# Optimization experiments

Measured on AMD Instinct MI355X. Metric: run time of the kernel, lower is better.

## Reference

```python
import jax, jax.numpy as jnp
import numpy as np
import math

N_HEAD = 16
N_KV_HEAD = 4
N_EMBD = 2048
HEAD_DIM = N_EMBD // N_HEAD  # 128
SCALE = 1.0 / math.sqrt(HEAD_DIM)
B, T = 2, 2048


def setup_inputs() -> dict:
    key = jax.random.key(0)
    ks = jax.random.split(key, 5)
    s = 0.02
    x = jax.random.normal(ks[0], (B, T, N_EMBD), dtype=jnp.float32)
    wq = jax.random.normal(ks[1], (N_EMBD, N_EMBD), dtype=jnp.float32) * s
    wk = jax.random.normal(ks[2], (N_KV_HEAD * HEAD_DIM, N_EMBD), dtype=jnp.float32) * s
    wv = jax.random.normal(ks[3], (N_KV_HEAD * HEAD_DIM, N_EMBD), dtype=jnp.float32) * s
    wo = jax.random.normal(ks[4], (N_EMBD, N_EMBD), dtype=jnp.float32) * s
    return {"x": x, "wq": wq, "wk": wk, "wv": wv, "wo": wo}


def _forward(x, wq, wk, wv, wo):
    b, t, _ = x.shape
    # Linear layers: y = x @ W.T  (torch Linear weight is (out,in))
    q = (x @ wq.T).reshape(b, t, N_HEAD, HEAD_DIM).transpose(0, 2, 1, 3)      # (B,H,T,D)
    k = (x @ wk.T).reshape(b, t, N_KV_HEAD, HEAD_DIM).transpose(0, 2, 1, 3)  # (B,Hkv,T,D)
    v = (x @ wv.T).reshape(b, t, N_KV_HEAD, HEAD_DIM).transpose(0, 2, 1, 3)
    groups = N_HEAD // N_KV_HEAD
    k = jnp.repeat(k, groups, axis=1)  # repeat_interleave over head dim -> (B,H,T,D)
    v = jnp.repeat(v, groups, axis=1)
    # Causal mask: True above diagonal (masked-out positions)
    mask = jnp.triu(jnp.ones((t, t), dtype=bool), k=1)[None, None]  # (1,1,T,T)
    scores = jnp.einsum('bhqd,bhkd->bhqk', q, k) * SCALE
    scores = jnp.where(mask, -jnp.inf, scores)
    attn = jax.nn.softmax(scores, axis=-1)
    attn = jnp.where(mask, 0.0, attn)
    y = jnp.einsum('bhqk,bhkd->bhqd', attn, v)       # (B,H,T,D)
    y = y.transpose(0, 2, 1, 3).reshape(b, t, N_EMBD)
    return y @ wo.T


def reference(x, wq, wk, wv, wo):
    return _forward(x, wq, wk, wv, wo)
```

## Files before the change

kernel.cpp:

```cpp
#include <hip/hip_runtime.h>
#include <cstdint>
#include <cstddef>

typedef __bf16 bf16_t;
typedef __bf16 bf16x8 __attribute__((ext_vector_type(8)));
typedef __bf16 bf16x4 __attribute__((ext_vector_type(4)));
typedef float f32x4 __attribute__((ext_vector_type(4)));

#define GL2LDS16(gptr, lptr)                                                   \
  __builtin_amdgcn_global_load_lds(                                            \
      (__attribute__((address_space(1))) void*)(gptr),                         \
      (__attribute__((address_space(3))) void*)(lptr), 16, 0, 0)

__device__ __forceinline__ float fast_exp2(float x) {
  float r;
  asm volatile("v_exp_f32 %0, %1" : "=v"(r) : "v"(x));
  return r;
}

#define BATCH 2
#define T_SEQ 2048
#define NH 16
#define NKV 4
#define HD 128
#define EMB 2048
#define KVDIM (NKV * HD)
#define MROWS (BATCH * T_SEQ)

__global__ void cvt_all(const float4* __restrict__ x,  const float4* __restrict__ wq,
                        const float4* __restrict__ wk, const float4* __restrict__ wv,
                        const float4* __restrict__ wo,
                        bf16x4* __restrict__ xb,  bf16x4* __restrict__ wqb,
                        bf16x4* __restrict__ wkb, bf16x4* __restrict__ wvb,
                        bf16x4* __restrict__ wob) {
  const int blk = blockIdx.x;
  const float4* src;
  bf16x4* dst;
  int base;
  if (blk < 8192)       { src = x;  dst = xb;  base = blk; }
  else if (blk < 12288) { src = wq; dst = wqb; base = blk - 8192; }
  else if (blk < 13312) { src = wk; dst = wkb; base = blk - 12288; }
  else if (blk < 14336) { src = wv; dst = wvb; base = blk - 13312; }
  else                  { src = wo; dst = wob; base = blk - 14336; }
  const int i = base * 256 + threadIdx.x;
  const float4 v = src[i];
  dst[i] = bf16x4{(__bf16)v.x, (__bf16)v.y, (__bf16)v.z, (__bf16)v.w};
}

__global__ __launch_bounds__(256, 2)
void gemm_qkv(const bf16_t* __restrict__ A,
              const bf16_t* __restrict__ Wq, const bf16_t* __restrict__ Wk,
              const bf16_t* __restrict__ Wv,
              bf16_t* __restrict__ Qb, bf16_t* __restrict__ Kb,
              bf16_t* __restrict__ Vt, float qalpha)
{
  __shared__ bf16_t As[128 * 64];
  __shared__ bf16_t Bs[128 * 64];

  const int tid  = threadIdx.x;
  const int lane = tid & 63;
  const int wv   = tid >> 6;
  const int nbx = blockIdx.x;
  const int m0 = blockIdx.y * 128;
  const int wm = (wv >> 1) * 64;
  const int wn = (wv & 1) * 64;
  const int l15 = lane & 15;
  const int lq  = lane >> 4;

  const bf16_t* Bm;
  int ncol0;
  if (nbx < 16)      { Bm = Wq; ncol0 = nbx * 128; }
  else if (nbx < 20) { Bm = Wk; ncol0 = (nbx - 16) * 128; }
  else               { Bm = Wv; ncol0 = (nbx - 20) * 128; }

  f32x4 acc[4][4] = {};
  const int srow = tid >> 3;
  const int scol = (tid & 7) * 8;

  for (int k0 = 0; k0 < EMB; k0 += 64) {
#pragma unroll
    for (int r = 0; r < 4; ++r) {
      const int row = r * 32 + srow;
      GL2LDS16(A + (size_t)(m0 + row) * EMB + k0 + scol, As + row * 64 + scol);
    }
#pragma unroll
    for (int r = 0; r < 4; ++r) {
      const int row = r * 32 + srow;
      GL2LDS16(Bm + (size_t)(ncol0 + row) * EMB + k0 + scol, Bs + row * 64 + scol);
    }
    __syncthreads();

#pragma unroll
    for (int ks = 0; ks < 2; ++ks) {
      const int kc = ks * 32 + lq * 8;
      bf16x8 af[4], bf[4];
#pragma unroll
      for (int i = 0; i < 4; ++i)
        af[i] = *(const bf16x8*)(As + (wm + i * 16 + l15) * 64 + kc);
#pragma unroll
      for (int j = 0; j < 4; ++j)
        bf[j] = *(const bf16x8*)(Bs + (wn + j * 16 + l15) * 64 + kc);
#pragma unroll
      for (int i = 0; i < 4; ++i)
#pragma unroll
        for (int j = 0; j < 4; ++j)
          acc[i][j] = __builtin_amdgcn_mfma_f32_16x16x32_bf16(af[i], bf[j], acc[i][j], 0, 0, 0);
    }
    __syncthreads();
  }

  if (nbx < 16) {
#pragma unroll
    for (int i = 0; i < 4; ++i) {
      const int rbase = m0 + wm + i * 16 + lq * 4;
#pragma unroll
      for (int j = 0; j < 4; ++j) {
        const int col = ncol0 + wn + j * 16 + l15;
#pragma unroll
        for (int r = 0; r < 4; ++r)
          Qb[(size_t)(rbase + r) * EMB + col] = (bf16_t)(acc[i][j][r] * qalpha);
      }
    }
  } else if (nbx < 20) {
#pragma unroll
    for (int i = 0; i < 4; ++i) {
      const int rbase = m0 + wm + i * 16 + lq * 4;
#pragma unroll
      for (int j = 0; j < 4; ++j) {
        const int col = ncol0 + wn + j * 16 + l15;
#pragma unroll
        for (int r = 0; r < 4; ++r)
          Kb[(size_t)(rbase + r) * KVDIM + col] = (bf16_t)acc[i][j][r];
      }
    }
  } else {
    const int b = m0 >> 11;
    const int mloc0 = (m0 & 2047) + wm + lq * 4;
#pragma unroll
    for (int i = 0; i < 4; ++i) {
      const int mloc = mloc0 + i * 16;
#pragma unroll
      for (int j = 0; j < 4; ++j) {
        const int d = ncol0 + wn + j * 16 + l15;
        *(bf16x4*)(Vt + (size_t)(b * KVDIM + d) * T_SEQ + mloc) =
            bf16x4{(__bf16)acc[i][j][0], (__bf16)acc[i][j][1],
                   (__bf16)acc[i][j][2], (__bf16)acc[i][j][3]};
      }
    }
  }
}

__global__ __launch_bounds__(256, 2)
void gemm_out(const bf16_t* __restrict__ A, const bf16_t* __restrict__ Bm,
              float* __restrict__ C, int M, int N, int K)
{
  __shared__ bf16_t As[128 * 64];
  __shared__ bf16_t Bs[128 * 64];

  const int tid  = threadIdx.x;
  const int lane = tid & 63;
  const int wv   = tid >> 6;
  const int m0 = blockIdx.y * 128;
  const int n0 = blockIdx.x * 128;
  const int wm = (wv >> 1) * 64;
  const int wn = (wv & 1) * 64;
  const int l15 = lane & 15;
  const int lq  = lane >> 4;

  f32x4 acc[4][4] = {};
  const int srow = tid >> 3;
  const int scol = (tid & 7) * 8;

  for (int k0 = 0; k0 < K; k0 += 64) {
#pragma unroll
    for (int r = 0; r < 4; ++r) {
      const int row = r * 32 + srow;
      GL2LDS16(A + (size_t)(m0 + row) * K + k0 + scol, As + row * 64 + scol);
    }
#pragma unroll
    for (int r = 0; r < 4; ++r) {
      const int row = r * 32 + srow;
      GL2LDS16(Bm + (size_t)(n0 + row) * K + k0 + scol, Bs + row * 64 + scol);
    }
    __syncthreads();

#pragma unroll
    for (int ks = 0; ks < 2; ++ks) {
      const int kc = ks * 32 + lq * 8;
      bf16x8 af[4], bf[4];
#pragma unroll
      for (int i = 0; i < 4; ++i)
        af[i] = *(const bf16x8*)(As + (wm + i * 16 + l15) * 64 + kc);
#pragma unroll
      for (int j = 0; j < 4; ++j)
        bf[j] = *(const bf16x8*)(Bs + (wn + j * 16 + l15) * 64 + kc);
#pragma unroll
      for (int i = 0; i < 4; ++i)
#pragma unroll
        for (int j = 0; j < 4; ++j)
          acc[i][j] = __builtin_amdgcn_mfma_f32_16x16x32_bf16(af[i], bf[j], acc[i][j], 0, 0, 0);
    }
    __syncthreads();
  }

#pragma unroll
  for (int i = 0; i < 4; ++i) {
    const int rbase = m0 + wm + i * 16 + lq * 4;
#pragma unroll
    for (int j = 0; j < 4; ++j) {
      const int col = n0 + wn + j * 16 + l15;
#pragma unroll
      for (int r = 0; r < 4; ++r)
        C[(size_t)(rbase + r) * N + col] = acc[i][j][r];
    }
  }
}

#define PSTR 72

__global__ __launch_bounds__(256, 2)
void attn_fwd(const bf16_t* __restrict__ Q, const bf16_t* __restrict__ Kg,
              const bf16_t* __restrict__ Vt, bf16_t* __restrict__ Y)
{
  __shared__ bf16_t Ks[2][64 * 128];
  __shared__ bf16_t Vs[2][128 * 64];
  __shared__ bf16_t Ps[4][16 * PSTR];

  const int tid  = threadIdx.x;
  const int lane = tid & 63;
  const int wv   = tid >> 6;
  const int l15  = lane & 15;
  const int lq   = lane >> 4;
  const int h  = blockIdx.y;
  const int b  = blockIdx.z;
  const int hkv = h >> 2;
  bf16_t* Psw = Ps[wv];

  auto stage = [&](int kt, int bufsel) {
    const int base_t = b * T_SEQ + kt * 64;
#pragma unroll
    for (int r = 0; r < 4; ++r) {
      const int c = r * 256 + tid;
      const int row = c >> 4, p = c & 15;
      const int sb = p ^ (row & 7);
      GL2LDS16(Kg + (size_t)(base_t + row) * KVDIM + hkv * HD + sb * 8,
               &Ks[bufsel][c * 8]);
    }
#pragma unroll
    for (int r = 0; r < 4; ++r) {
      const int c = r * 256 + tid;
      const int row = c >> 3, p = c & 7;
      const int sb = p ^ (row & 7);
      GL2LDS16(Vt + (size_t)(b * KVDIM + hkv * HD + row) * T_SEQ + kt * 64 + sb * 8,
               &Vs[bufsel][c * 8]);
    }
  };

#pragma unroll 1
  for (int ph = 0; ph < 2; ++ph) {
    const int qt = ph ? blockIdx.x : (31 - blockIdx.x);
    const int q0 = qt * 64;
    const int nkt = qt + 1;
    const int qabs = q0 + wv * 16 + l15;

    bf16x8 qf[4];
    {
      const bf16_t* qp = Q + ((size_t)(b * T_SEQ + qabs) * NH + h) * HD + lq * 8;
#pragma unroll
      for (int ds = 0; ds < 4; ++ds)
        qf[ds] = *(const bf16x8*)(qp + ds * 32);
    }

    float l_part = 0.f;
    f32x4 o[8];
#pragma unroll
    for (int nb = 0; nb < 8; ++nb) o[nb] = f32x4{0.f, 0.f, 0.f, 0.f};

    __syncthreads();
    stage(0, 0);

    for (int kt = 0; kt < nkt; ++kt) {
      const int cur = kt & 1;
      __syncthreads();
      if (kt + 1 < nkt) stage(kt + 1, cur ^ 1);

      f32x4 s[4];
#pragma unroll
      for (int nb = 0; nb < 4; ++nb) {
        s[nb] = f32x4{0.f, 0.f, 0.f, 0.f};
        const int row = nb * 16 + l15;
        const int r7  = row & 7;
#pragma unroll
        for (int ds = 0; ds < 4; ++ds) {
          const bf16x8 kf = *(const bf16x8*)&Ks[cur][row * 128 + (((ds * 4 + lq) ^ r7) * 8)];
          s[nb] = __builtin_amdgcn_mfma_f32_16x16x32_bf16(kf, qf[ds], s[nb], 0, 0, 0);
        }
      }

      const bool dia = (kt == nkt - 1);
#pragma unroll
      for (int nb = 0; nb < 4; ++nb) {
        const int kvb = kt * 64 + nb * 16 + lq * 4;
        float p0, p1, p2, p3;
        if (dia) {
          p0 = (kvb + 0 <= qabs) ? fast_exp2(s[nb][0]) : 0.f;
          p1 = (kvb + 1 <= qabs) ? fast_exp2(s[nb][1]) : 0.f;
          p2 = (kvb + 2 <= qabs) ? fast_exp2(s[nb][2]) : 0.f;
          p3 = (kvb + 3 <= qabs) ? fast_exp2(s[nb][3]) : 0.f;
        } else {
          p0 = fast_exp2(s[nb][0]);
          p1 = fast_exp2(s[nb][1]);
          p2 = fast_exp2(s[nb][2]);
          p3 = fast_exp2(s[nb][3]);
        }
        l_part += (p0 + p1) + (p2 + p3);
        *(bf16x4*)(Psw + l15 * PSTR + nb * 16 + lq * 4) =
            bf16x4{(__bf16)p0, (__bf16)p1, (__bf16)p2, (__bf16)p3};
      }

      asm volatile("s_waitcnt lgkmcnt(0)" ::: "memory");

#pragma unroll
      for (int ks = 0; ks < 2; ++ks) {
        const bf16x8 pf = *(const bf16x8*)(Psw + l15 * PSTR + ks * 32 + lq * 8);
#pragma unroll
        for (int nb = 0; nb < 8; ++nb) {
          const int row = nb * 16 + l15;
          const bf16x8 vf = *(const bf16x8*)&Vs[cur][row * 64 + (((ks * 4 + lq) ^ (row & 7)) * 8)];
          o[nb] = __builtin_amdgcn_mfma_f32_16x16x32_bf16(vf, pf, o[nb], 0, 0, 0);
        }
      }
    }

    float lt = l_part;
    lt += __shfl_xor(lt, 16);
    lt += __shfl_xor(lt, 32);
    const float inv = 1.f / lt;
    bf16_t* yp = Y + ((size_t)(b * T_SEQ + qabs) * NH + h) * HD + lq * 4;
#pragma unroll
    for (int nb = 0; nb < 8; ++nb) {
      *(bf16x4*)(yp + nb * 16) = bf16x4{(__bf16)(o[nb][0] * inv), (__bf16)(o[nb][1] * inv),
                                        (__bf16)(o[nb][2] * inv), (__bf16)(o[nb][3] * inv)};
    }
  }
}

extern "C" void kernel_launch(void* const* d_in, const int* in_sizes, int n_in,
                              void* d_out, int out_size, void* d_ws, size_t ws_size,
                              hipStream_t stream) {
  const float* x  = (const float*)d_in[0];
  const float* wq = (const float*)d_in[1];
  const float* wk = (const float*)d_in[2];
  const float* wv = (const float*)d_in[3];
  const float* wo = (const float*)d_in[4];
  float* out = (float*)d_out;

  const size_t n_x  = (size_t)MROWS * EMB;
  const size_t n_wq = (size_t)EMB * EMB;
  const size_t n_wk = (size_t)KVDIM * EMB;

  bf16_t* xb  = (bf16_t*)d_ws;
  bf16_t* wqb = xb  + n_x;
  bf16_t* wkb = wqb + n_wq;
  bf16_t* wvb = wkb + n_wk;
  bf16_t* wob = wvb + n_wk;
  bf16_t* Qb  = wob + n_wq;
  bf16_t* Kb  = Qb + (size_t)MROWS * EMB;
  bf16_t* Vtb = Kb + (size_t)MROWS * KVDIM;
  bf16_t* Yb  = Vtb + (size_t)MROWS * KVDIM;

  dim3 blk(256);

  cvt_all<<<dim3(18432), blk, 0, stream>>>(
      (const float4*)x, (const float4*)wq, (const float4*)wk, (const float4*)wv, (const float4*)wo,
      (bf16x4*)xb, (bf16x4*)wqb, (bf16x4*)wkb, (bf16x4*)wvb, (bf16x4*)wob);

  const float qalpha = 0.08838834764831845f * 1.4426950408889634f;
  gemm_qkv<<<dim3(24, MROWS / 128), blk, 0, stream>>>(xb, wqb, wkb, wvb,
                                                      Qb, Kb, Vtb, qalpha);

  attn_fwd<<<dim3(16, NH, BATCH), blk, 0, stream>>>(Qb, Kb, Vtb, Yb);

  gemm_out<<<dim3(EMB / 128, MROWS / 128), blk, 0, stream>>>(Yb, wob, out, MROWS, EMB, EMB);
}
```

Before: 283.3 us.

## Rewrite QKV GEMM as 256x256 8-wave double-buffered pipelined kernel

Replaces the 128x128, 4-wave QKV projection GEMM with a 256x256 tile, 512-thread kernel. It double-buffers LDS with direct global-to-LDS loads interleaved between MFMA phases, XOR-swizzles the LDS layout to avoid bank conflicts, raises wave priority around MFMA bursts, and remaps block IDs for better L2 locality. The goal is to hide global load latency and raise data reuse per tile. In exchange it uses 128KB of LDS per block and many more accumulator registers, which can limit occupancy. The hand-placed vmcnt waits are fragile.

```diff
diff --git a/kernel.cpp b/kernel.cpp
--- a/kernel.cpp
+++ b/kernel.cpp
@@ -47,71 +47,157 @@
   dst[i] = bf16x4{(__bf16)v.x, (__bf16)v.y, (__bf16)v.z, (__bf16)v.w};
 }
 
-__global__ __launch_bounds__(256, 2)
-void gemm_qkv(const bf16_t* __restrict__ A,
-              const bf16_t* __restrict__ Wq, const bf16_t* __restrict__ Wk,
-              const bf16_t* __restrict__ Wv,
-              bf16_t* __restrict__ Qb, bf16_t* __restrict__ Kb,
-              bf16_t* __restrict__ Vt, float qalpha)
+#define BK8 64
+#define NT8 (EMB / BK8)
+
+__global__ __launch_bounds__(512, 2)
+void gemm_qkv8(const bf16_t* __restrict__ A,
+               const bf16_t* __restrict__ Wq, const bf16_t* __restrict__ Wk,
+               const bf16_t* __restrict__ Wv,
+               bf16_t* __restrict__ Qb, bf16_t* __restrict__ Kb,
+               bf16_t* __restrict__ Vt, float qalpha)
 {
-  __shared__ bf16_t As[128 * 64];
-  __shared__ bf16_t Bs[128 * 64];
+  __shared__ bf16_t lds[2][512 * 64];
 
   const int tid  = threadIdx.x;
   const int lane = tid & 63;
   const int wv   = tid >> 6;
-  const int nbx = blockIdx.x;
-  const int m0 = blockIdx.y * 128;
-  const int wm = (wv >> 1) * 64;
-  const int wn = (wv & 1) * 64;
-  const int l15 = lane & 15;
-  const int lq  = lane >> 4;
-
-  const bf16_t* Bm;
-  int ncol0;
-  if (nbx < 16)      { Bm = Wq; ncol0 = nbx * 128; }
-  else if (nbx < 20) { Bm = Wk; ncol0 = (nbx - 16) * 128; }
-  else               { Bm = Wv; ncol0 = (nbx - 20) * 128; }
-
-  f32x4 acc[4][4] = {};
-  const int srow = tid >> 3;
-  const int scol = (tid & 7) * 8;
-
-  for (int k0 = 0; k0 < EMB; k0 += 64) {
-#pragma unroll
-    for (int r = 0; r < 4; ++r) {
-      const int row = r * 32 + srow;
-      GL2LDS16(A + (size_t)(m0 + row) * EMB + k0 + scol, As + row * 64 + scol);
-    }
-#pragma unroll
-    for (int r = 0; r < 4; ++r) {
-      const int row = r * 32 + srow;
-      GL2LDS16(Bm + (size_t)(ncol0 + row) * EMB + k0 + scol, Bs + row * 64 + scol);
-    }
-    __syncthreads();
-
-#pragma unroll
-    for (int ks = 0; ks < 2; ++ks) {
-      const int kc = ks * 32 + lq * 8;
-      bf16x8 af[4], bf[4];
-#pragma unroll
-      for (int i = 0; i < 4; ++i)
-        af[i] = *(const bf16x8*)(As + (wm + i * 16 + l15) * 64 + kc);
-#pragma unroll
-      for (int j = 0; j < 4; ++j)
-        bf[j] = *(const bf16x8*)(Bs + (wn + j * 16 + l15) * 64 + kc);
-#pragma unroll
-      for (int i = 0; i < 4; ++i)
-#pragma unroll
-        for (int j = 0; j < 4; ++j)
-          acc[i][j] = __builtin_amdgcn_mfma_f32_16x16x32_bf16(af[i], bf[j], acc[i][j], 0, 0, 0);
-    }
-    __syncthreads();
+  const int l15  = lane & 15;
+  const int lq   = lane >> 4;
+
+  const int bid0 = blockIdx.x;
+  const int bid  = (bid0 & 7) * 24 + (bid0 >> 3);
+  const int mt = bid / 12, nt = bid % 12;
+  const int m0 = mt * 256;
+
+  const bf16_t* Bmat; int ncol0, seg;
+  if (nt < 8)       { Bmat = Wq; ncol0 = nt * 256;        seg = 0; }
+  else if (nt < 10) { Bmat = Wk; ncol0 = (nt - 8) * 256;  seg = 1; }
+  else              { Bmat = Wv; ncol0 = (nt - 10) * 256; seg = 2; }
+
+  const int wm = (wv >> 2) * 128;
+  const int wn = (wv & 3) * 64;
+
+  f32x4 acc[8][4] = {};
+
+  auto stage = [&](int dbuf, int tsrc, int h) {
+    const int k0 = tsrc * BK8;
+    const bf16_t* src = (h < 2) ? A : Bmat;
+    const int rbase = (h < 2) ? (m0 + h * 128) : (ncol0 + (h - 2) * 128);
+    bf16_t* dst = &lds[dbuf][h * 8192];
+#pragma unroll
+    for (int r = 0; r < 2; ++r) {
+      const int c = r * 512 + tid;
+      const int row = c >> 3, p = c & 7;
+      const int sb = p ^ (row & 7);
+      GL2LDS16(src + (size_t)(rbase + row) * EMB + k0 + sb * 8, dst + c * 8);
+    }
+  };
+
+  stage(0, 0, 0); stage(0, 0, 1); stage(0, 0, 2); stage(0, 0, 3);
+  stage(1, 1, 2); stage(1, 1, 0); stage(1, 1, 3);
+  asm volatile("s_waitcnt vmcnt(6)" ::: "memory");
+  __builtin_amdgcn_s_barrier();
+
+  bf16x8 a[4][2], b[4][2];
+
+#pragma unroll 1
+  for (int tt = 0; tt < NT8; tt += 2) {
+#pragma unroll
+    for (int u = 0; u < 2; ++u) {
+      const int t   = tt + u;
+      const int cur = u;
+      const int nxt = u ^ 1;
+      const int tn1 = (t + 1 < NT8) ? t + 1 : NT8 - 1;
+      const int tn2 = (t + 2 < NT8) ? t + 2 : NT8 - 1;
+
+#pragma unroll
+      for (int i = 0; i < 4; ++i) {
+        const int row = wm + i * 16 + l15;
+#pragma unroll
+        for (int ks = 0; ks < 2; ++ks)
+          a[i][ks] = *(const bf16x8*)&lds[cur][row * 64 + (((ks * 4 + lq) ^ (row & 7)) * 8)];
+      }
+#pragma unroll
+      for (int j = 0; j < 2; ++j) {
+        const int row = 256 + wn + j * 16 + l15;
+#pragma unroll
+        for (int ks = 0; ks < 2; ++ks)
+          b[j][ks] = *(const bf16x8*)&lds[cur][row * 64 + (((ks * 4 + lq) ^ (row & 7)) * 8)];
+      }
+      stage(nxt, tn1, 1);
+      __builtin_amdgcn_s_barrier();
+      __builtin_amdgcn_s_setprio(1);
+#pragma unroll
+      for (int ks = 0; ks < 2; ++ks)
+#pragma unroll
+        for (int i = 0; i < 4; ++i)
+#pragma unroll
+          for (int j = 0; j < 2; ++j)
+            acc[i][j] = __builtin_amdgcn_mfma_f32_16x16x32_bf16(a[i][ks], b[j][ks], acc[i][j], 0, 0, 0);
+      __builtin_amdgcn_s_setprio(0);
+      __builtin_amdgcn_s_barrier();
+
+#pragma unroll
+      for (int j = 2; j < 4; ++j) {
+        const int row = 256 + wn + j * 16 + l15;
+#pragma unroll
+        for (int ks = 0; ks < 2; ++ks)
+          b[j][ks] = *(const bf16x8*)&lds[cur][row * 64 + (((ks * 4 + lq) ^ (row & 7)) * 8)];
+      }
+      __builtin_amdgcn_s_barrier();
+      __builtin_amdgcn_s_setprio(1);
+#pragma unroll
+      for (int ks = 0; ks < 2; ++ks)
+#pragma unroll
+        for (int i = 0; i < 4; ++i)
+#pragma unroll
+          for (int j = 2; j < 4; ++j)
+            acc[i][j] = __builtin_amdgcn_mfma_f32_16x16x32_bf16(a[i][ks], b[j][ks], acc[i][j], 0, 0, 0);
+      __builtin_amdgcn_s_setprio(0);
+      __builtin_amdgcn_s_barrier();
+
+#pragma unroll
+      for (int i = 0; i < 4; ++i) {
+        const int row = wm + (4 + i) * 16 + l15;
+#pragma unroll
+        for (int ks = 0; ks < 2; ++ks)
+          a[i][ks] = *(const bf16x8*)&lds[cur][row * 64 + (((ks * 4 + lq) ^ (row & 7)) * 8)];
+      }
+      stage(cur, tn2, 2);
+      __builtin_amdgcn_s_barrier();
+      __builtin_amdgcn_s_setprio(1);
+#pragma unroll
+      for (int ks = 0; ks < 2; ++ks)
+#pragma unroll
+        for (int i = 0; i < 4; ++i)
+#pragma unroll
+          for (int j = 2; j < 4; ++j)
+            acc[4 + i][j] = __builtin_amdgcn_mfma_f32_16x16x32_bf16(a[i][ks], b[j][ks], acc[4 + i][j], 0, 0, 0);
+      __builtin_amdgcn_s_setprio(0);
+      __builtin_amdgcn_s_barrier();
+
+      stage(cur, tn2, 0);
+      stage(cur, tn2, 3);
+      __builtin_amdgcn_s_barrier();
+      __builtin_amdgcn_s_setprio(1);
+#pragma unroll
+      for (int ks = 0; ks < 2; ++ks)
+#pragma unroll
+        for (int i = 0; i < 4; ++i)
+#pragma unroll
+          for (int j = 0; j < 2; ++j)
+            acc[4 + i][j] = __builtin_amdgcn_mfma_f32_16x16x32_bf16(a[i][ks], b[j][ks], acc[4 + i][j], 0, 0, 0);
+      __builtin_amdgcn_s_setprio(0);
+      asm volatile("s_waitcnt vmcnt(6)" ::: "memory");
+      __builtin_amdgcn_s_barrier();
+    }
   }
-
-  if (nbx < 16) {
-#pragma unroll
-    for (int i = 0; i < 4; ++i) {
+  asm volatile("s_waitcnt vmcnt(0)" ::: "memory");
+
+  if (seg == 0) {
+#pragma unroll
+    for (int i = 0; i < 8; ++i) {
       const int rbase = m0 + wm + i * 16 + lq * 4;
 #pragma unroll
       for (int j = 0; j < 4; ++j) {
@@ -121,9 +207,9 @@
           Qb[(size_t)(rbase + r) * EMB + col] = (bf16_t)(acc[i][j][r] * qalpha);
       }
     }
-  } else if (nbx < 20) {
-#pragma unroll
-    for (int i = 0; i < 4; ++i) {
+  } else if (seg == 1) {
+#pragma unroll
+    for (int i = 0; i < 8; ++i) {
       const int rbase = m0 + wm + i * 16 + lq * 4;
 #pragma unroll
       for (int j = 0; j < 4; ++j) {
@@ -134,15 +220,15 @@
       }
     }
   } else {
-    const int b = m0 >> 11;
+    const int bb = m0 >> 11;
     const int mloc0 = (m0 & 2047) + wm + lq * 4;
 #pragma unroll
-    for (int i = 0; i < 4; ++i) {
+    for (int i = 0; i < 8; ++i) {
       const int mloc = mloc0 + i * 16;
 #pragma unroll
       for (int j = 0; j < 4; ++j) {
         const int d = ncol0 + wn + j * 16 + l15;
-        *(bf16x4*)(Vt + (size_t)(b * KVDIM + d) * T_SEQ + mloc) =
+        *(bf16x4*)(Vt + (size_t)(bb * KVDIM + d) * T_SEQ + mloc) =
             bf16x4{(__bf16)acc[i][j][0], (__bf16)acc[i][j][1],
                    (__bf16)acc[i][j][2], (__bf16)acc[i][j][3]};
       }
@@ -376,8 +462,8 @@
       (bf16x4*)xb, (bf16x4*)wqb, (bf16x4*)wkb, (bf16x4*)wvb, (bf16x4*)wob);
 
   const float qalpha = 0.08838834764831845f * 1.4426950408889634f;
-  gemm_qkv<<<dim3(24, MROWS / 128), blk, 0, stream>>>(xb, wqb, wkb, wvb,
-                                                      Qb, Kb, Vtb, qalpha);
+  gemm_qkv8<<<dim3(192), dim3(512), 0, stream>>>(xb, wqb, wkb, wvb,
+                                                 Qb, Kb, Vtb, qalpha);
 
   attn_fwd<<<dim3(16, NH, BATCH), blk, 0, stream>>>(Qb, Kb, Vtb, Yb);
 
```

Result: no change. 278.9 us (-1.6%).
